# Performance work log

Hardware: AMD Instinct MI355X
Metric: run time of the kernel (lower is better)

Reference implementation:

```python
import jax, jax.numpy as jnp
import numpy as np
import math

B, L, E, H = 512, 200, 64, 4
D = E // H
NEG = jnp.float32(-(2.0 ** 32) + 1.0)


def setup_inputs() -> dict:
    key = jax.random.key(0)
    ks = jax.random.split(key, 12)
    inp = jax.random.normal(ks[0], (B, L, E), dtype=jnp.float32)
    # realistic variable-length histories: mask[b, t] = t < len_b, len_b in [1, L]
    lens = jax.random.randint(ks[1], (B, 1), 1, L + 1)
    mask = jnp.arange(L)[None, :] < lens  # [B, L] bool
    s = 1.0 / math.sqrt(E)
    pos_enc = jax.random.normal(ks[2], (1, L, E), dtype=jnp.float32)
    Wk = jax.random.uniform(ks[3], (E, E), jnp.float32, -s, s)
    bk = jnp.zeros((E,), jnp.float32)
    Wv = jax.random.uniform(ks[4], (E, E), jnp.float32, -s, s)
    bv = jnp.zeros((E,), jnp.float32)
    Wq = jax.random.uniform(ks[5], (E, E), jnp.float32, -s, s)
    bq = jnp.zeros((E,), jnp.float32)
    Wf = jax.random.uniform(ks[6], (E, E), jnp.float32, -s, s)
    bf = jnp.zeros((E,), jnp.float32)
    return {"input": inp, "mask": mask, "pos_enc": pos_enc,
            "Wk": Wk, "bk": bk, "Wv": Wv, "bv": bv,
            "Wq": Wq, "bq": bq, "Wf": Wf, "bf": bf}


def reference(input, mask, pos_enc, Wk, bk, Wv, bv, Wq, bq, Wf, bf):
    x = input + pos_enc  # [B, L, E]
    # project and split heads: [B, H, L, D]
    def split(t):
        return t.reshape(B, L, H, D).transpose(0, 2, 1, 3)
    k = split(x @ Wk.T + bk)
    v = split(x @ Wv.T + bv)
    q = split(x @ Wq.T + bq) / math.sqrt(D)
    scores = jnp.einsum('bhqd,bhkd->bhqk', q, k)  # [B, H, L, L]
    # key_mask in torch code broadcasts over dim 3 (mask on the QUERY axis),
    # query_mask is its transpose (mask on the KEY axis). Combined: both must be valid.
    both = mask[:, None, :, None] & mask[:, None, None, :]  # [B, 1, L, L]
    scores = jnp.where(both, scores, NEG)
    attn = jax.nn.softmax(scores, axis=-1)
    # dropout is identity at inference; omitted deterministically
    out = jnp.einsum('bhqk,bhkd->bhqd', attn, v)
    out = out.transpose(0, 2, 1, 3).reshape(B, L, E)
    out = out @ Wf.T + bf
    fm = mask.astype(jnp.float32)[:, :, None]  # [B, L, 1]
    lens = jnp.sum(fm, axis=1)  # [B, 1]
    pooled = jnp.sum(out * fm, axis=1) / (lens + 1e-8)  # [B, E]
    return pooled
```

## Files before the change

### kernel.cpp

```cpp
#include <hip/hip_runtime.h>
#include <hip/hip_fp16.h>
#include <math.h>

#define Bn 512
#define Ln 200
#define En 64
#define Hn 4
#define Dn 16
#define KS3 18
#define VS3 200
#define QSC 0.36067376022224085f

typedef _Float16 __f16;
typedef __fp16 fp16x2 __attribute__((ext_vector_type(2)));
typedef __f16 f16x4 __attribute__((ext_vector_type(4)));
typedef __f16 f16x8 __attribute__((ext_vector_type(8)));
typedef float f32x4 __attribute__((ext_vector_type(4)));

#if __has_builtin(__builtin_amdgcn_exp2f)
__device__ __forceinline__ float fexp2(float x) { return __builtin_amdgcn_exp2f(x); }
#else
__device__ __forceinline__ float fexp2(float x) { return exp2f(x); }
#endif

__device__ __forceinline__ f16x8 pack8s(float4 a, float4 b, float4 pa, float4 pb) {
    f16x8 r;
    r[0] = (__f16)(a.x + pa.x); r[1] = (__f16)(a.y + pa.y);
    r[2] = (__f16)(a.z + pa.z); r[3] = (__f16)(a.w + pa.w);
    r[4] = (__f16)(b.x + pb.x); r[5] = (__f16)(b.y + pb.y);
    r[6] = (__f16)(b.z + pb.z); r[7] = (__f16)(b.w + pb.w);
    return r;
}
__device__ __forceinline__ f16x8 pack8(float4 a, float4 b) {
    f16x8 r;
    r[0] = (__f16)a.x; r[1] = (__f16)a.y; r[2] = (__f16)a.z; r[3] = (__f16)a.w;
    r[4] = (__f16)b.x; r[5] = (__f16)b.y; r[6] = (__f16)b.z; r[7] = (__f16)b.w;
    return r;
}

__device__ __forceinline__ f16x4 pack4rtz(float e0, float e1, float e2, float e3) {
    const fp16x2 lo = __builtin_amdgcn_cvt_pkrtz(e0, e1);
    const fp16x2 hi = __builtin_amdgcn_cvt_pkrtz(e2, e3);
    f16x4 r;
    r[0] = (__f16)lo[0]; r[1] = (__f16)lo[1];
    r[2] = (__f16)hi[0]; r[3] = (__f16)hi[1];
    return r;
}

template<int NI>
__device__ __forceinline__ void attn_core(
    const __f16* __restrict__ Kh_, const __f16* __restrict__ Qh_, const __f16* __restrict__ Vt_,
    int qt0, int klo, int khi, int nt, int len, int quad, int ln16,
    f32x4 (&o2)[4], f32x4 (&lacc)[4])
{
    const f16x4 ones = {(__f16)1.f, (__f16)1.f, (__f16)1.f, (__f16)1.f};
    f16x4 qf[NI];
    #pragma unroll
    for (int i = 0; i < NI; ++i) {
        int qr = min((qt0 + i) * 16 + ln16, Ln - 1);
        qf[i] = *(const f16x4*)(Qh_ + qr * KS3 + quad * 4);
    }
    const bool needmask = (khi == nt);
    const int kfull = khi - (needmask ? 1 : 0);

    f16x4 kf = *(const f16x4*)(Kh_ + min(klo * 16 + ln16, Ln - 1) * KS3 + quad * 4);
    f16x4 vf = *(const f16x4*)(Vt_ + ln16 * VS3 + min(klo * 16 + quad * 4, Ln - 4));

    for (int kt = klo; kt < kfull; ++kt) {
        const int krn = min((kt + 1) * 16 + ln16, Ln - 1);
        const int vcn = min((kt + 1) * 16 + quad * 4, Ln - 4);
        const f16x4 kfn = *(const f16x4*)(Kh_ + krn * KS3 + quad * 4);
        const f16x4 vfn = *(const f16x4*)(Vt_ + ln16 * VS3 + vcn);
        f32x4 s[NI];
        #pragma unroll
        for (int i = 0; i < NI; ++i)
            s[i] = __builtin_amdgcn_mfma_f32_16x16x16f16(kf, qf[i], (f32x4){0,0,0,0}, 0, 0, 0);
        f16x4 pf[NI];
        #pragma unroll
        for (int i = 0; i < NI; ++i) {
            pf[i] = pack4rtz(fexp2(fminf(s[i][0], 14.5f)),
                             fexp2(fminf(s[i][1], 14.5f)),
                             fexp2(fminf(s[i][2], 14.5f)),
                             fexp2(fminf(s[i][3], 14.5f)));
        }
        #pragma unroll
        for (int i = 0; i < NI; ++i) {
            o2[i]   = __builtin_amdgcn_mfma_f32_16x16x16f16(vf,   pf[i], o2[i],   0, 0, 0);
            lacc[i] = __builtin_amdgcn_mfma_f32_16x16x16f16(ones, pf[i], lacc[i], 0, 0, 0);
        }
        kf = kfn; vf = vfn;
    }
    if (needmask) {
        const int kbase = (nt - 1) * 16 + quad * 4;
        f32x4 s[NI];
        #pragma unroll
        for (int i = 0; i < NI; ++i)
            s[i] = __builtin_amdgcn_mfma_f32_16x16x16f16(kf, qf[i], (f32x4){0,0,0,0}, 0, 0, 0);
        f16x4 pf[NI];
        #pragma unroll
        for (int i = 0; i < NI; ++i) {
            float e[4];
            #pragma unroll
            for (int j = 0; j < 4; ++j) {
                const bool kok = (kbase + j) < len;
                e[j] = kok ? fexp2(fminf(s[i][j], 14.5f)) : 0.f;
            }
            pf[i] = pack4rtz(e[0], e[1], e[2], e[3]);
        }
        #pragma unroll
        for (int i = 0; i < NI; ++i) {
            o2[i]   = __builtin_amdgcn_mfma_f32_16x16x16f16(vf,   pf[i], o2[i],   0, 0, 0);
            lacc[i] = __builtin_amdgcn_mfma_f32_16x16x16f16(ones, pf[i], lacc[i], 0, 0, 0);
        }
    }
}

__global__ __launch_bounds__(256, 4) void fused_kernel(
    const float* __restrict__ input, const int* __restrict__ mask,
    const float* __restrict__ pos_enc,
    const float* __restrict__ Wk, const float* __restrict__ bk,
    const float* __restrict__ Wv, const float* __restrict__ bv,
    const float* __restrict__ Wq, const float* __restrict__ bq,
    const float* __restrict__ Wf, const float* __restrict__ bf_,
    float* __restrict__ out)
{
    __shared__ __align__(16) __f16 Kh[Ln * KS3];
    __shared__ __align__(16) __f16 Qh[Ln * KS3];
    __shared__ __align__(16) __f16 Vt[16 * VS3];
    __shared__ float lred[4][4][16];
    __shared__ float red[4][16];
    __shared__ float ph[16];
    __shared__ int cnt_red[4];

    const int tid  = threadIdx.x;
    const int lin  = ((blockIdx.x & 7) << 8) | (blockIdx.x >> 3);
    const int b    = lin >> 2, h = lin & 3;
    const int wave = tid >> 6, lane = tid & 63;
    const int quad = lane >> 4, ln16 = lane & 15;

    const float4* in4 = (const float4*)(input + (size_t)b * Ln * En);
    const float4* pe4 = (const float4*)pos_enc;

    float4 px0, px1, px2, px3;
    {
        const int o4 = (wave * 16 + ln16) * 16 + quad * 2;
        px0 = in4[o4];     px1 = in4[o4 + 1];
        px2 = in4[o4 + 8]; px3 = in4[o4 + 9];
    }

    const int mv = (tid < Ln) ? mask[b * Ln + tid] : 0;

    f16x8 bfr[3][2];
    #pragma unroll
    for (int m = 0; m < 3; ++m) {
        const float* W = (m == 0) ? Wk : (m == 1) ? Wv : Wq;
        #pragma unroll
        for (int ks = 0; ks < 2; ++ks) {
            const float4* wp = (const float4*)(W + (size_t)(h * 16 + ln16) * 64) + (ks * 8 + quad * 2);
            bfr[m][ks] = pack8(wp[0], wp[1]);
        }
    }
    const int cg = h * 16 + ln16;
    const float bkv = bk[cg], bvv = bv[cg], bqv = bq[cg];

    int c = (mv != 0) ? 1 : 0;
    #pragma unroll
    for (int off = 32; off; off >>= 1) c += __shfl_down(c, off, 64);
    if (lane == 0) cnt_red[wave] = c;
    __syncthreads();
    const int len = cnt_red[0] + cnt_red[1] + cnt_red[2] + cnt_red[3];
    const int nt = (len + 15) >> 4;

    for (int rt = wave; rt < nt; rt += 4) {
        const int R = rt * 16 + ln16;
        const bool rok = (R < Ln);
        const int o4 = R * 16 + quad * 2;

        const int rtn = rt + 4;
        const int Rn = rtn * 16 + ln16;
        float4 pxn0 = {0,0,0,0}, pxn1 = {0,0,0,0}, pxn2 = {0,0,0,0}, pxn3 = {0,0,0,0};
        if (rtn < nt && Rn < Ln) {
            const int o4n = Rn * 16 + quad * 2;
            pxn0 = in4[o4n];     pxn1 = in4[o4n + 1];
            pxn2 = in4[o4n + 8]; pxn3 = in4[o4n + 9];
        }
        float4 pp0 = {0,0,0,0}, pp1 = {0,0,0,0}, pp2 = {0,0,0,0}, pp3 = {0,0,0,0};
        if (rok) {
            pp0 = pe4[o4];     pp1 = pe4[o4 + 1];
            pp2 = pe4[o4 + 8]; pp3 = pe4[o4 + 9];
        }
        f16x8 af0 = pack8s(px0, px1, pp0, pp1);
        f16x8 af1 = pack8s(px2, px3, pp2, pp3);

        f32x4 acc[3];
        #pragma unroll
        for (int m = 0; m < 3; ++m) acc[m] = (f32x4){0,0,0,0};
        #pragma unroll
        for (int m = 0; m < 3; ++m)
            acc[m] = __builtin_amdgcn_mfma_f32_16x16x32_f16(af0, bfr[m][0], acc[m], 0, 0, 0);
        #pragma unroll
        for (int m = 0; m < 3; ++m)
            acc[m] = __builtin_amdgcn_mfma_f32_16x16x32_f16(af1, bfr[m][1], acc[m], 0, 0, 0);

        #pragma unroll
        for (int j = 0; j < 4; ++j) {
            const int t = rt * 16 + quad * 4 + j;
            if (t < Ln) {
                Kh[t * KS3 + ln16] = (__f16)(acc[0][j] + bkv);
                Qh[t * KS3 + ln16] = (__f16)((acc[2][j] + bqv) * QSC);
            }
        }
        const int vc0 = rt * 16 + quad * 4;
        if (vc0 < Ln) {
            f16x4 vp;
            #pragma unroll
            for (int j = 0; j < 4; ++j) vp[j] = (__f16)(acc[1][j] + bvv);
            *(f16x4*)(Vt + ln16 * VS3 + vc0) = vp;
        }
        px0 = pxn0; px1 = pxn1; px2 = pxn2; px3 = pxn3;
    }
    __syncthreads();

    const int nquad = (nt + 3) >> 2;
    int g, kh, nkh;
    if (nquad >= 3)      { g = wave;     kh = 0;         nkh = 1; }
    else if (nquad == 2) { g = wave & 1; kh = wave >> 1; nkh = 2; }
    else                 { g = 0;        kh = wave;      nkh = 4; }
    const bool active = (g < nquad);
    const int nktp = (nt + nkh - 1) / nkh;
    const int klo = kh * nktp;
    const int khi = min(klo + nktp, nt);
    const int qt0 = 4 * g;

    f32x4 o2[4], lacc[4];
    #pragma unroll
    for (int i = 0; i < 4; ++i) { o2[i] = (f32x4){0,0,0,0}; lacc[i] = (f32x4){0,0,0,0}; }

    if (active && klo < khi) {
        const int ni = __builtin_amdgcn_readfirstlane(min(4, nt - qt0));
        switch (ni) {
            case 1:  attn_core<1>(Kh, Qh, Vt, qt0, klo, khi, nt, len, quad, ln16, o2, lacc); break;
            case 2:  attn_core<2>(Kh, Qh, Vt, qt0, klo, khi, nt, len, quad, ln16, o2, lacc); break;
            case 3:  attn_core<3>(Kh, Qh, Vt, qt0, klo, khi, nt, len, quad, ln16, o2, lacc); break;
            default: attn_core<4>(Kh, Qh, Vt, qt0, klo, khi, nt, len, quad, ln16, o2, lacc); break;
        }
    }

    float l[4];
    #pragma unroll
    for (int i = 0; i < 4; ++i) l[i] = lacc[i][0];

    if (nkh > 1) {
        if (lane < 16) {
            #pragma unroll
            for (int i = 0; i < 4; ++i) lred[wave][i][lane] = l[i];
        }
        __syncthreads();
        #pragma unroll
        for (int i = 0; i < 4; ++i) {
            if (nkh == 2) l[i] = lred[g][i][ln16] + lred[g + 2][i][ln16];
            else          l[i] = lred[0][i][ln16] + lred[1][i][ln16]
                               + lred[2][i][ln16] + lred[3][i][ln16];
        }
    }

    f32x4 pool = {0.f, 0.f, 0.f, 0.f};
    if (active) {
        #pragma unroll
        for (int i = 0; i < 4; ++i) {
            const float rs = ((qt0 + i) * 16 + ln16 < len) ? 1.f / l[i] : 0.f;
            #pragma unroll
            for (int j = 0; j < 4; ++j) pool[j] = fmaf(o2[i][j], rs, pool[j]);
        }
    }

    #pragma unroll
    for (int j = 0; j < 4; ++j) {
        #pragma unroll
        for (int off = 1; off < 16; off <<= 1) pool[j] += __shfl_xor(pool[j], off, 64);
    }
    if (ln16 == 0) {
        #pragma unroll
        for (int j = 0; j < 4; ++j) red[wave][quad * 4 + j] = pool[j];
    }
    __syncthreads();
    if (tid < 16)
        ph[tid] = (red[0][tid] + red[1][tid] + red[2][tid] + red[3][tid]) / ((float)len + 1e-8f);
    __syncthreads();

    if (tid < 64) {
        const int e = tid;
        const float* wr = Wf + (size_t)e * 64 + h * 16;
        float a = (h == 0) ? bf_[e] : 0.f;
        #pragma unroll
        for (int i = 0; i < 16; ++i) a = fmaf(wr[i], ph[i], a);
        atomicAdd(out + b * En + e, a);
    }
}

extern "C" void kernel_launch(void* const* d_in, const int* in_sizes, int n_in,
                              void* d_out, int out_size, void* d_ws, size_t ws_size,
                              hipStream_t stream) {
    const float* input   = (const float*)d_in[0];
    const int*   mask    = (const int*)  d_in[1];
    const float* pos_enc = (const float*)d_in[2];
    const float* Wk      = (const float*)d_in[3];
    const float* bk      = (const float*)d_in[4];
    const float* Wv      = (const float*)d_in[5];
    const float* bv      = (const float*)d_in[6];
    const float* Wq      = (const float*)d_in[7];
    const float* bq      = (const float*)d_in[8];
    const float* Wf      = (const float*)d_in[9];
    const float* bf      = (const float*)d_in[10];

    float* out = (float*)d_out;
    hipMemsetAsync(out, 0, (size_t)Bn * En * sizeof(float), stream);

    fused_kernel<<<Bn * Hn, 256, 0, stream>>>(input, mask, pos_enc,
                                              Wk, bk, Wv, bv, Wq, bq, Wf, bf, out);
}
```

Baseline: 122.0 us.

## Use persistent 512-thread blocks with atomic ticket work queue over (batch, head) items

Replaces the one-block-per-(batch,head) launch with 1024 persistent blocks of 8 waves that pull work items from a global atomic ticket counter. The projection loop now strides over 8 waves and attention splits key ranges across more waves, with the l-reduction always going through shared memory. The intent is to balance the very uneven per-item work caused by variable sequence lengths and to use more waves per item. In exchange it adds an atomic plus extra barriers per item, a second memset for the ticket, and possible occupancy limits from launch_bounds(512,8).

```diff
diff --git a/kernel.cpp b/kernel.cpp
--- a/kernel.cpp
+++ b/kernel.cpp
@@ -6,7 +6,7 @@
 #define Ln 200
 #define En 64
 #define Hn 4
-#define Dn 16
+#define NITEMS (Bn * Hn)
 #define KS3 18
 #define VS3 200
 #define QSC 0.36067376022224085f
@@ -115,186 +115,210 @@
     }
 }
 
-__global__ __launch_bounds__(256, 4) void fused_kernel(
+__global__ __launch_bounds__(512, 8) void fused_kernel(
     const float* __restrict__ input, const int* __restrict__ mask,
     const float* __restrict__ pos_enc,
     const float* __restrict__ Wk, const float* __restrict__ bk,
     const float* __restrict__ Wv, const float* __restrict__ bv,
     const float* __restrict__ Wq, const float* __restrict__ bq,
     const float* __restrict__ Wf, const float* __restrict__ bf_,
-    float* __restrict__ out)
+    float* __restrict__ out, int* __restrict__ ticket)
 {
     __shared__ __align__(16) __f16 Kh[Ln * KS3];
     __shared__ __align__(16) __f16 Qh[Ln * KS3];
     __shared__ __align__(16) __f16 Vt[16 * VS3];
-    __shared__ float lred[4][4][16];
-    __shared__ float red[4][16];
+    __shared__ float lred[8][4][16];
+    __shared__ float red[8][16];
     __shared__ float ph[16];
-    __shared__ int cnt_red[4];
+    __shared__ int cnt_red[8];
+    __shared__ int item_sh;
 
     const int tid  = threadIdx.x;
-    const int lin  = ((blockIdx.x & 7) << 8) | (blockIdx.x >> 3);
-    const int b    = lin >> 2, h = lin & 3;
     const int wave = tid >> 6, lane = tid & 63;
     const int quad = lane >> 4, ln16 = lane & 15;
-
-    const float4* in4 = (const float4*)(input + (size_t)b * Ln * En);
     const float4* pe4 = (const float4*)pos_enc;
 
-    float4 px0, px1, px2, px3;
-    {
-        const int o4 = (wave * 16 + ln16) * 16 + quad * 2;
-        px0 = in4[o4];     px1 = in4[o4 + 1];
-        px2 = in4[o4 + 8]; px3 = in4[o4 + 9];
-    }
-
-    const int mv = (tid < Ln) ? mask[b * Ln + tid] : 0;
-
-    f16x8 bfr[3][2];
-    #pragma unroll
-    for (int m = 0; m < 3; ++m) {
-        const float* W = (m == 0) ? Wk : (m == 1) ? Wv : Wq;
-        #pragma unroll
-        for (int ks = 0; ks < 2; ++ks) {
-            const float4* wp = (const float4*)(W + (size_t)(h * 16 + ln16) * 64) + (ks * 8 + quad * 2);
-            bfr[m][ks] = pack8(wp[0], wp[1]);
-        }
-    }
-    const int cg = h * 16 + ln16;
-    const float bkv = bk[cg], bvv = bv[cg], bqv = bq[cg];
-
-    int c = (mv != 0) ? 1 : 0;
-    #pragma unroll
-    for (int off = 32; off; off >>= 1) c += __shfl_down(c, off, 64);
-    if (lane == 0) cnt_red[wave] = c;
-    __syncthreads();
-    const int len = cnt_red[0] + cnt_red[1] + cnt_red[2] + cnt_red[3];
-    const int nt = (len + 15) >> 4;
-
-    for (int rt = wave; rt < nt; rt += 4) {
-        const int R = rt * 16 + ln16;
-        const bool rok = (R < Ln);
-        const int o4 = R * 16 + quad * 2;
-
-        const int rtn = rt + 4;
-        const int Rn = rtn * 16 + ln16;
-        float4 pxn0 = {0,0,0,0}, pxn1 = {0,0,0,0}, pxn2 = {0,0,0,0}, pxn3 = {0,0,0,0};
-        if (rtn < nt && Rn < Ln) {
-            const int o4n = Rn * 16 + quad * 2;
-            pxn0 = in4[o4n];     pxn1 = in4[o4n + 1];
-            pxn2 = in4[o4n + 8]; pxn3 = in4[o4n + 9];
-        }
-        float4 pp0 = {0,0,0,0}, pp1 = {0,0,0,0}, pp2 = {0,0,0,0}, pp3 = {0,0,0,0};
-        if (rok) {
-            pp0 = pe4[o4];     pp1 = pe4[o4 + 1];
-            pp2 = pe4[o4 + 8]; pp3 = pe4[o4 + 9];
-        }
-        f16x8 af0 = pack8s(px0, px1, pp0, pp1);
-        f16x8 af1 = pack8s(px2, px3, pp2, pp3);
-
-        f32x4 acc[3];
-        #pragma unroll
-        for (int m = 0; m < 3; ++m) acc[m] = (f32x4){0,0,0,0};
-        #pragma unroll
-        for (int m = 0; m < 3; ++m)
-            acc[m] = __builtin_amdgcn_mfma_f32_16x16x32_f16(af0, bfr[m][0], acc[m], 0, 0, 0);
-        #pragma unroll
-        for (int m = 0; m < 3; ++m)
-            acc[m] = __builtin_amdgcn_mfma_f32_16x16x32_f16(af1, bfr[m][1], acc[m], 0, 0, 0);
+    for (;;) {
+        __syncthreads();
+        if (tid == 0) item_sh = atomicAdd(ticket, 1);
+        __syncthreads();
+        const int item = item_sh;
+        if (item >= NITEMS) break;
+        const int b = item >> 2, h = item & 3;
+
+        const float4* in4 = (const float4*)(input + (size_t)b * Ln * En);
+
+        float4 px0 = {0,0,0,0}, px1 = {0,0,0,0}, px2 = {0,0,0,0}, px3 = {0,0,0,0};
+        if (wave == 0) {
+            const int o4 = ln16 * 16 + quad * 2;
+            px0 = in4[o4];     px1 = in4[o4 + 1];
+            px2 = in4[o4 + 8]; px3 = in4[o4 + 9];
+        }
+
+        const int mv = (tid < Ln) ? mask[b * Ln + tid] : 0;
+
+        f16x8 bfr[3][2];
+        #pragma unroll
+        for (int m = 0; m < 3; ++m) {
+            const float* W = (m == 0) ? Wk : (m == 1) ? Wv : Wq;
+            #pragma unroll
+            for (int ks = 0; ks < 2; ++ks) {
+                const float4* wp = (const float4*)(W + (size_t)(h * 16 + ln16) * 64) + (ks * 8 + quad * 2);
+                bfr[m][ks] = pack8(wp[0], wp[1]);
+            }
+        }
+        const int cg = h * 16 + ln16;
+        const float bkv = bk[cg], bvv = bv[cg], bqv = bq[cg];
+
+        int c = (mv != 0) ? 1 : 0;
+        #pragma unroll
+        for (int off = 32; off; off >>= 1) c += __shfl_down(c, off, 64);
+        if (lane == 0) cnt_red[wave] = c;
+        __syncthreads();
+        int len = 0;
+        #pragma unroll
+        for (int w = 0; w < 8; ++w) len += cnt_red[w];
+        const int nt = (len + 15) >> 4;
+
+        if (wave != 0 && wave < nt) {
+            const int o4 = (wave * 16 + ln16) * 16 + quad * 2;
+            px0 = in4[o4];     px1 = in4[o4 + 1];
+            px2 = in4[o4 + 8]; px3 = in4[o4 + 9];
+        }
+
+        for (int rt = wave; rt < nt; rt += 8) {
+            const int R = rt * 16 + ln16;
+            const bool rok = (R < Ln);
+            const int o4 = R * 16 + quad * 2;
+
+            const int rtn = rt + 8;
+            const int Rn = rtn * 16 + ln16;
+            float4 pxn0 = {0,0,0,0}, pxn1 = {0,0,0,0}, pxn2 = {0,0,0,0}, pxn3 = {0,0,0,0};
+            if (rtn < nt && Rn < Ln) {
+                const int o4n = Rn * 16 + quad * 2;
+                pxn0 = in4[o4n];     pxn1 = in4[o4n + 1];
+                pxn2 = in4[o4n + 8]; pxn3 = in4[o4n + 9];
+            }
+            float4 pp0 = {0,0,0,0}, pp1 = {0,0,0,0}, pp2 = {0,0,0,0}, pp3 = {0,0,0,0};
+            if (rok) {
+                pp0 = pe4[o4];     pp1 = pe4[o4 + 1];
+                pp2 = pe4[o4 + 8]; pp3 = pe4[o4 + 9];
+            }
+            const f16x8 af0 = pack8s(px0, px1, pp0, pp1);
+            const f16x8 af1 = pack8s(px2, px3, pp2, pp3);
+
+            f32x4 acc[3];
+            #pragma unroll
+            for (int m = 0; m < 3; ++m) acc[m] = (f32x4){0,0,0,0};
+            #pragma unroll
+            for (int m = 0; m < 3; ++m)
+                acc[m] = __builtin_amdgcn_mfma_f32_16x16x32_f16(af0, bfr[m][0], acc[m], 0, 0, 0);
+            #pragma unroll
+            for (int m = 0; m < 3; ++m)
+                acc[m] = __builtin_amdgcn_mfma_f32_16x16x32_f16(af1, bfr[m][1], acc[m], 0, 0, 0);
+
+            #pragma unroll
+            for (int j = 0; j < 4; ++j) {
+                const int t = rt * 16 + quad * 4 + j;
+                if (t < Ln) {
+                    Kh[t * KS3 + ln16] = (__f16)(acc[0][j] + bkv);
+                    Qh[t * KS3 + ln16] = (__f16)((acc[2][j] + bqv) * QSC);
+                }
+            }
+            const int vc0 = rt * 16 + quad * 4;
+            if (vc0 < Ln) {
+                f16x4 vp;
+                #pragma unroll
+                for (int j = 0; j < 4; ++j) vp[j] = (__f16)(acc[1][j] + bvv);
+                *(f16x4*)(Vt + ln16 * VS3 + vc0) = vp;
+            }
+            px0 = pxn0; px1 = pxn1; px2 = pxn2; px3 = pxn3;
+        }
+        __syncthreads();
+
+        const int nquad = (nt + 3) >> 2;
+        int g, kh, nkh;
+        if (nquad >= 3)      { g = wave & 3; kh = wave >> 2; nkh = 2; }
+        else if (nquad == 2) { g = wave & 1; kh = wave >> 1; nkh = 4; }
+        else                 { g = 0;        kh = wave;      nkh = 8; }
+        const bool active = (g < nquad);
+        const int nktp = (nt + nkh - 1) / nkh;
+        const int klo = kh * nktp;
+        const int khi = min(klo + nktp, nt);
+        const int qt0 = 4 * g;
+
+        f32x4 o2[4], lacc[4];
+        #pragma unroll
+        for (int i = 0; i < 4; ++i) { o2[i] = (f32x4){0,0,0,0}; lacc[i] = (f32x4){0,0,0,0}; }
+
+        if (active && klo < khi) {
+            const int ni = __builtin_amdgcn_readfirstlane(min(4, nt - qt0));
+            switch (ni) {
+                case 1:  attn_core<1>(Kh, Qh, Vt, qt0, klo, khi, nt, len, quad, ln16, o2, lacc); break;
+                case 2:  attn_core<2>(Kh, Qh, Vt, qt0, klo, khi, nt, len, quad, ln16, o2, lacc); break;
+                case 3:  attn_core<3>(Kh, Qh, Vt, qt0, klo, khi, nt, len, quad, ln16, o2, lacc); break;
+                default: attn_core<4>(Kh, Qh, Vt, qt0, klo, khi, nt, len, quad, ln16, o2, lacc); break;
+            }
+        }
+
+        float l[4];
+        #pragma unroll
+        for (int i = 0; i < 4; ++i) l[i] = lacc[i][0];
+
+        if (lane < 16) {
+            #pragma unroll
+            for (int i = 0; i < 4; ++i) lred[wave][i][lane] = l[i];
+        }
+        __syncthreads();
+        #pragma unroll
+        for (int i = 0; i < 4; ++i) {
+            if (nkh == 2)      l[i] = lred[g][i][ln16] + lred[g + 4][i][ln16];
+            else if (nkh == 4) l[i] = lred[g][i][ln16] + lred[g + 2][i][ln16]
+                                    + lred[g + 4][i][ln16] + lred[g + 6][i][ln16];
+            else {
+                float s = 0.f;
+                #pragma unroll
+                for (int w = 0; w < 8; ++w) s += lred[w][i][ln16];
+                l[i] = s;
+            }
+        }
+
+        f32x4 pool = {0.f, 0.f, 0.f, 0.f};
+        if (active) {
+            #pragma unroll
+            for (int i = 0; i < 4; ++i) {
+                const float rs = ((qt0 + i) * 16 + ln16 < len) ? 1.f / l[i] : 0.f;
+                #pragma unroll
+                for (int j = 0; j < 4; ++j) pool[j] = fmaf(o2[i][j], rs, pool[j]);
+            }
+        }
 
         #pragma unroll
         for (int j = 0; j < 4; ++j) {
-            const int t = rt * 16 + quad * 4 + j;
-            if (t < Ln) {
-                Kh[t * KS3 + ln16] = (__f16)(acc[0][j] + bkv);
-                Qh[t * KS3 + ln16] = (__f16)((acc[2][j] + bqv) * QSC);
-            }
-        }
-        const int vc0 = rt * 16 + quad * 4;
-        if (vc0 < Ln) {
-            f16x4 vp;
-            #pragma unroll
-            for (int j = 0; j < 4; ++j) vp[j] = (__f16)(acc[1][j] + bvv);
-            *(f16x4*)(Vt + ln16 * VS3 + vc0) = vp;
-        }
-        px0 = pxn0; px1 = pxn1; px2 = pxn2; px3 = pxn3;
-    }
-    __syncthreads();
-
-    const int nquad = (nt + 3) >> 2;
-    int g, kh, nkh;
-    if (nquad >= 3)      { g = wave;     kh = 0;         nkh = 1; }
-    else if (nquad == 2) { g = wave & 1; kh = wave >> 1; nkh = 2; }
-    else                 { g = 0;        kh = wave;      nkh = 4; }
-    const bool active = (g < nquad);
-    const int nktp = (nt + nkh - 1) / nkh;
-    const int klo = kh * nktp;
-    const int khi = min(klo + nktp, nt);
-    const int qt0 = 4 * g;
-
-    f32x4 o2[4], lacc[4];
-    #pragma unroll
-    for (int i = 0; i < 4; ++i) { o2[i] = (f32x4){0,0,0,0}; lacc[i] = (f32x4){0,0,0,0}; }
-
-    if (active && klo < khi) {
-        const int ni = __builtin_amdgcn_readfirstlane(min(4, nt - qt0));
-        switch (ni) {
-            case 1:  attn_core<1>(Kh, Qh, Vt, qt0, klo, khi, nt, len, quad, ln16, o2, lacc); break;
-            case 2:  attn_core<2>(Kh, Qh, Vt, qt0, klo, khi, nt, len, quad, ln16, o2, lacc); break;
-            case 3:  attn_core<3>(Kh, Qh, Vt, qt0, klo, khi, nt, len, quad, ln16, o2, lacc); break;
-            default: attn_core<4>(Kh, Qh, Vt, qt0, klo, khi, nt, len, quad, ln16, o2, lacc); break;
-        }
-    }
-
-    float l[4];
-    #pragma unroll
-    for (int i = 0; i < 4; ++i) l[i] = lacc[i][0];
-
-    if (nkh > 1) {
-        if (lane < 16) {
-            #pragma unroll
-            for (int i = 0; i < 4; ++i) lred[wave][i][lane] = l[i];
-        }
-        __syncthreads();
-        #pragma unroll
-        for (int i = 0; i < 4; ++i) {
-            if (nkh == 2) l[i] = lred[g][i][ln16] + lred[g + 2][i][ln16];
-            else          l[i] = lred[0][i][ln16] + lred[1][i][ln16]
-                               + lred[2][i][ln16] + lred[3][i][ln16];
-        }
-    }
-
-    f32x4 pool = {0.f, 0.f, 0.f, 0.f};
-    if (active) {
-        #pragma unroll
-        for (int i = 0; i < 4; ++i) {
-            const float rs = ((qt0 + i) * 16 + ln16 < len) ? 1.f / l[i] : 0.f;
-            #pragma unroll
-            for (int j = 0; j < 4; ++j) pool[j] = fmaf(o2[i][j], rs, pool[j]);
-        }
-    }
-
-    #pragma unroll
-    for (int j = 0; j < 4; ++j) {
-        #pragma unroll
-        for (int off = 1; off < 16; off <<= 1) pool[j] += __shfl_xor(pool[j], off, 64);
-    }
-    if (ln16 == 0) {
-        #pragma unroll
-        for (int j = 0; j < 4; ++j) red[wave][quad * 4 + j] = pool[j];
-    }
-    __syncthreads();
-    if (tid < 16)
-        ph[tid] = (red[0][tid] + red[1][tid] + red[2][tid] + red[3][tid]) / ((float)len + 1e-8f);
-    __syncthreads();
-
-    if (tid < 64) {
-        const int e = tid;
-        const float* wr = Wf + (size_t)e * 64 + h * 16;
-        float a = (h == 0) ? bf_[e] : 0.f;
-        #pragma unroll
-        for (int i = 0; i < 16; ++i) a = fmaf(wr[i], ph[i], a);
-        atomicAdd(out + b * En + e, a);
+            #pragma unroll
+            for (int off = 1; off < 16; off <<= 1) pool[j] += __shfl_xor(pool[j], off, 64);
+        }
+        if (ln16 == 0) {
+            #pragma unroll
+            for (int j = 0; j < 4; ++j) red[wave][quad * 4 + j] = pool[j];
+        }
+        __syncthreads();
+        if (tid < 16) {
+            float s = 0.f;
+            #pragma unroll
+            for (int w = 0; w < 8; ++w) s += red[w][tid];
+            ph[tid] = s / ((float)len + 1e-8f);
+        }
+        __syncthreads();
+
+        if (tid < 64) {
+            const int e = tid;
+            const float* wr = Wf + (size_t)e * 64 + h * 16;
+            float a = (h == 0) ? bf_[e] : 0.f;
+            #pragma unroll
+            for (int i = 0; i < 16; ++i) a = fmaf(wr[i], ph[i], a);
+            atomicAdd(out + b * En + e, a);
+        }
     }
 }
 
@@ -313,9 +337,13 @@
     const float* Wf      = (const float*)d_in[9];
     const float* bf      = (const float*)d_in[10];
 
-    float* out = (float*)d_out;
+    float* out    = (float*)d_out;
+    int*   ticket = (int*)d_ws;
+
     hipMemsetAsync(out, 0, (size_t)Bn * En * sizeof(float), stream);
-
-    fused_kernel<<<Bn * Hn, 256, 0, stream>>>(input, mask, pos_enc,
-                                              Wk, bk, Wv, bv, Wq, bq, Wf, bf, out);
-}
+    hipMemsetAsync(ticket, 0, 64, stream);
+
+    fused_kernel<<<1024, 512, 0, stream>>>(input, mask, pos_enc,
+                                           Wk, bk, Wv, bv, Wq, bq, Wf, bf,
+                                           out, ticket);
+}
```

Result: slower. 214.7 us (+76.0%).

## Convert to persistent blocks pulling (batch, head) items from an atomic ticket

Applied to the files above, without the earlier changes.

Replaces the one-block-per-(batch,head) grid with a fixed grid of 1792 persistent blocks. Each block repeatedly grabs a work item through an atomic counter in workspace, which is zeroed by an extra memset. Dynamic scheduling is meant to balance the uneven per-item cost from variable sequence lengths and to cut block launch overhead. Input prefetch for waves beyond the valid tile count is now deferred until the length is known. The cost is an extra memset, a global atomic and barrier per item, and an extra trailing barrier per iteration.

```diff
diff --git a/kernel.cpp b/kernel.cpp
--- a/kernel.cpp
+++ b/kernel.cpp
@@ -6,7 +6,7 @@
 #define Ln 200
 #define En 64
 #define Hn 4
-#define Dn 16
+#define NITEMS (Bn * Hn)
 #define KS3 18
 #define VS3 200
 #define QSC 0.36067376022224085f
@@ -122,7 +122,7 @@
     const float* __restrict__ Wv, const float* __restrict__ bv,
     const float* __restrict__ Wq, const float* __restrict__ bq,
     const float* __restrict__ Wf, const float* __restrict__ bf_,
-    float* __restrict__ out)
+    float* __restrict__ out, int* __restrict__ ticket)
 {
     __shared__ __align__(16) __f16 Kh[Ln * KS3];
     __shared__ __align__(16) __f16 Qh[Ln * KS3];
@@ -131,170 +131,184 @@
     __shared__ float red[4][16];
     __shared__ float ph[16];
     __shared__ int cnt_red[4];
+    __shared__ int item_sh;
 
     const int tid  = threadIdx.x;
-    const int lin  = ((blockIdx.x & 7) << 8) | (blockIdx.x >> 3);
-    const int b    = lin >> 2, h = lin & 3;
     const int wave = tid >> 6, lane = tid & 63;
     const int quad = lane >> 4, ln16 = lane & 15;
-
-    const float4* in4 = (const float4*)(input + (size_t)b * Ln * En);
     const float4* pe4 = (const float4*)pos_enc;
 
-    float4 px0, px1, px2, px3;
-    {
-        const int o4 = (wave * 16 + ln16) * 16 + quad * 2;
-        px0 = in4[o4];     px1 = in4[o4 + 1];
-        px2 = in4[o4 + 8]; px3 = in4[o4 + 9];
-    }
-
-    const int mv = (tid < Ln) ? mask[b * Ln + tid] : 0;
-
-    f16x8 bfr[3][2];
-    #pragma unroll
-    for (int m = 0; m < 3; ++m) {
-        const float* W = (m == 0) ? Wk : (m == 1) ? Wv : Wq;
-        #pragma unroll
-        for (int ks = 0; ks < 2; ++ks) {
-            const float4* wp = (const float4*)(W + (size_t)(h * 16 + ln16) * 64) + (ks * 8 + quad * 2);
-            bfr[m][ks] = pack8(wp[0], wp[1]);
-        }
-    }
-    const int cg = h * 16 + ln16;
-    const float bkv = bk[cg], bvv = bv[cg], bqv = bq[cg];
-
-    int c = (mv != 0) ? 1 : 0;
-    #pragma unroll
-    for (int off = 32; off; off >>= 1) c += __shfl_down(c, off, 64);
-    if (lane == 0) cnt_red[wave] = c;
-    __syncthreads();
-    const int len = cnt_red[0] + cnt_red[1] + cnt_red[2] + cnt_red[3];
-    const int nt = (len + 15) >> 4;
-
-    for (int rt = wave; rt < nt; rt += 4) {
-        const int R = rt * 16 + ln16;
-        const bool rok = (R < Ln);
-        const int o4 = R * 16 + quad * 2;
-
-        const int rtn = rt + 4;
-        const int Rn = rtn * 16 + ln16;
-        float4 pxn0 = {0,0,0,0}, pxn1 = {0,0,0,0}, pxn2 = {0,0,0,0}, pxn3 = {0,0,0,0};
-        if (rtn < nt && Rn < Ln) {
-            const int o4n = Rn * 16 + quad * 2;
-            pxn0 = in4[o4n];     pxn1 = in4[o4n + 1];
-            pxn2 = in4[o4n + 8]; pxn3 = in4[o4n + 9];
-        }
-        float4 pp0 = {0,0,0,0}, pp1 = {0,0,0,0}, pp2 = {0,0,0,0}, pp3 = {0,0,0,0};
-        if (rok) {
-            pp0 = pe4[o4];     pp1 = pe4[o4 + 1];
-            pp2 = pe4[o4 + 8]; pp3 = pe4[o4 + 9];
-        }
-        f16x8 af0 = pack8s(px0, px1, pp0, pp1);
-        f16x8 af1 = pack8s(px2, px3, pp2, pp3);
-
-        f32x4 acc[3];
-        #pragma unroll
-        for (int m = 0; m < 3; ++m) acc[m] = (f32x4){0,0,0,0};
-        #pragma unroll
-        for (int m = 0; m < 3; ++m)
-            acc[m] = __builtin_amdgcn_mfma_f32_16x16x32_f16(af0, bfr[m][0], acc[m], 0, 0, 0);
-        #pragma unroll
-        for (int m = 0; m < 3; ++m)
-            acc[m] = __builtin_amdgcn_mfma_f32_16x16x32_f16(af1, bfr[m][1], acc[m], 0, 0, 0);
+    for (;;) {
+        if (tid == 0) item_sh = atomicAdd(ticket, 1);
+        __syncthreads();
+        const int item = item_sh;
+        if (item >= NITEMS) break;
+        const int b = item >> 2, h = item & 3;
+
+        const float4* in4 = (const float4*)(input + (size_t)b * Ln * En);
+
+        float4 px0 = {0,0,0,0}, px1 = {0,0,0,0}, px2 = {0,0,0,0}, px3 = {0,0,0,0};
+        if (wave == 0) {
+            const int o4 = ln16 * 16 + quad * 2;
+            px0 = in4[o4];     px1 = in4[o4 + 1];
+            px2 = in4[o4 + 8]; px3 = in4[o4 + 9];
+        }
+
+        const int mv = (tid < Ln) ? mask[b * Ln + tid] : 0;
+
+        f16x8 bfr[3][2];
+        #pragma unroll
+        for (int m = 0; m < 3; ++m) {
+            const float* W = (m == 0) ? Wk : (m == 1) ? Wv : Wq;
+            #pragma unroll
+            for (int ks = 0; ks < 2; ++ks) {
+                const float4* wp = (const float4*)(W + (size_t)(h * 16 + ln16) * 64) + (ks * 8 + quad * 2);
+                bfr[m][ks] = pack8(wp[0], wp[1]);
+            }
+        }
+        const int cg = h * 16 + ln16;
+        const float bkv = bk[cg], bvv = bv[cg], bqv = bq[cg];
+
+        int c = (mv != 0) ? 1 : 0;
+        #pragma unroll
+        for (int off = 32; off; off >>= 1) c += __shfl_down(c, off, 64);
+        if (lane == 0) cnt_red[wave] = c;
+        __syncthreads();
+        const int len = cnt_red[0] + cnt_red[1] + cnt_red[2] + cnt_red[3];
+        const int nt = (len + 15) >> 4;
+
+        if (wave != 0 && wave < nt) {
+            const int o4 = (wave * 16 + ln16) * 16 + quad * 2;
+            px0 = in4[o4];     px1 = in4[o4 + 1];
+            px2 = in4[o4 + 8]; px3 = in4[o4 + 9];
+        }
+
+        for (int rt = wave; rt < nt; rt += 4) {
+            const int R = rt * 16 + ln16;
+            const bool rok = (R < Ln);
+            const int o4 = R * 16 + quad * 2;
+
+            const int rtn = rt + 4;
+            const int Rn = rtn * 16 + ln16;
+            float4 pxn0 = {0,0,0,0}, pxn1 = {0,0,0,0}, pxn2 = {0,0,0,0}, pxn3 = {0,0,0,0};
+            if (rtn < nt && Rn < Ln) {
+                const int o4n = Rn * 16 + quad * 2;
+                pxn0 = in4[o4n];     pxn1 = in4[o4n + 1];
+                pxn2 = in4[o4n + 8]; pxn3 = in4[o4n + 9];
+            }
+            float4 pp0 = {0,0,0,0}, pp1 = {0,0,0,0}, pp2 = {0,0,0,0}, pp3 = {0,0,0,0};
+            if (rok) {
+                pp0 = pe4[o4];     pp1 = pe4[o4 + 1];
+                pp2 = pe4[o4 + 8]; pp3 = pe4[o4 + 9];
+            }
+            const f16x8 af0 = pack8s(px0, px1, pp0, pp1);
+            const f16x8 af1 = pack8s(px2, px3, pp2, pp3);
+
+            f32x4 acc[3];
+            #pragma unroll
+            for (int m = 0; m < 3; ++m) acc[m] = (f32x4){0,0,0,0};
+            #pragma unroll
+            for (int m = 0; m < 3; ++m)
+                acc[m] = __builtin_amdgcn_mfma_f32_16x16x32_f16(af0, bfr[m][0], acc[m], 0, 0, 0);
+            #pragma unroll
+            for (int m = 0; m < 3; ++m)
+                acc[m] = __builtin_amdgcn_mfma_f32_16x16x32_f16(af1, bfr[m][1], acc[m], 0, 0, 0);
+
+            #pragma unroll
+            for (int j = 0; j < 4; ++j) {
+                const int t = rt * 16 + quad * 4 + j;
+                if (t < Ln) {
+                    Kh[t * KS3 + ln16] = (__f16)(acc[0][j] + bkv);
+                    Qh[t * KS3 + ln16] = (__f16)((acc[2][j] + bqv) * QSC);
+                }
+            }
+            const int vc0 = rt * 16 + quad * 4;
+            if (vc0 < Ln) {
+                f16x4 vp;
+                #pragma unroll
+                for (int j = 0; j < 4; ++j) vp[j] = (__f16)(acc[1][j] + bvv);
+                *(f16x4*)(Vt + ln16 * VS3 + vc0) = vp;
+            }
+            px0 = pxn0; px1 = pxn1; px2 = pxn2; px3 = pxn3;
+        }
+        __syncthreads();
+
+        const int nquad = (nt + 3) >> 2;
+        int g, kh, nkh;
+        if (nquad >= 3)      { g = wave;     kh = 0;         nkh = 1; }
+        else if (nquad == 2) { g = wave & 1; kh = wave >> 1; nkh = 2; }
+        else                 { g = 0;        kh = wave;      nkh = 4; }
+        const bool active = (g < nquad);
+        const int nktp = (nt + nkh - 1) / nkh;
+        const int klo = kh * nktp;
+        const int khi = min(klo + nktp, nt);
+        const int qt0 = 4 * g;
+
+        f32x4 o2[4], lacc[4];
+        #pragma unroll
+        for (int i = 0; i < 4; ++i) { o2[i] = (f32x4){0,0,0,0}; lacc[i] = (f32x4){0,0,0,0}; }
+
+        if (active && klo < khi) {
+            const int ni = __builtin_amdgcn_readfirstlane(min(4, nt - qt0));
+            switch (ni) {
+                case 1:  attn_core<1>(Kh, Qh, Vt, qt0, klo, khi, nt, len, quad, ln16, o2, lacc); break;
+                case 2:  attn_core<2>(Kh, Qh, Vt, qt0, klo, khi, nt, len, quad, ln16, o2, lacc); break;
+                case 3:  attn_core<3>(Kh, Qh, Vt, qt0, klo, khi, nt, len, quad, ln16, o2, lacc); break;
+                default: attn_core<4>(Kh, Qh, Vt, qt0, klo, khi, nt, len, quad, ln16, o2, lacc); break;
+            }
+        }
+
+        float l[4];
+        #pragma unroll
+        for (int i = 0; i < 4; ++i) l[i] = lacc[i][0];
+
+        if (nkh > 1) {
+            if (lane < 16) {
+                #pragma unroll
+                for (int i = 0; i < 4; ++i) lred[wave][i][lane] = l[i];
+            }
+            __syncthreads();
+            #pragma unroll
+            for (int i = 0; i < 4; ++i) {
+                if (nkh == 2) l[i] = lred[g][i][ln16] + lred[g + 2][i][ln16];
+                else          l[i] = lred[0][i][ln16] + lred[1][i][ln16]
+                                   + lred[2][i][ln16] + lred[3][i][ln16];
+            }
+        }
+
+        f32x4 pool = {0.f, 0.f, 0.f, 0.f};
+        if (active) {
+            #pragma unroll
+            for (int i = 0; i < 4; ++i) {
+                const float rs = ((qt0 + i) * 16 + ln16 < len) ? 1.f / l[i] : 0.f;
+                #pragma unroll
+                for (int j = 0; j < 4; ++j) pool[j] = fmaf(o2[i][j], rs, pool[j]);
+            }
+        }
 
         #pragma unroll
         for (int j = 0; j < 4; ++j) {
-            const int t = rt * 16 + quad * 4 + j;
-            if (t < Ln) {
-                Kh[t * KS3 + ln16] = (__f16)(acc[0][j] + bkv);
-                Qh[t * KS3 + ln16] = (__f16)((acc[2][j] + bqv) * QSC);
-            }
-        }
-        const int vc0 = rt * 16 + quad * 4;
-        if (vc0 < Ln) {
-            f16x4 vp;
-            #pragma unroll
-            for (int j = 0; j < 4; ++j) vp[j] = (__f16)(acc[1][j] + bvv);
-            *(f16x4*)(Vt + ln16 * VS3 + vc0) = vp;
-        }
-        px0 = pxn0; px1 = pxn1; px2 = pxn2; px3 = pxn3;
-    }
-    __syncthreads();
-
-    const int nquad = (nt + 3) >> 2;
-    int g, kh, nkh;
-    if (nquad >= 3)      { g = wave;     kh = 0;         nkh = 1; }
-    else if (nquad == 2) { g = wave & 1; kh = wave >> 1; nkh = 2; }
-    else                 { g = 0;        kh = wave;      nkh = 4; }
-    const bool active = (g < nquad);
-    const int nktp = (nt + nkh - 1) / nkh;
-    const int klo = kh * nktp;
-    const int khi = min(klo + nktp, nt);
-    const int qt0 = 4 * g;
-
-    f32x4 o2[4], lacc[4];
-    #pragma unroll
-    for (int i = 0; i < 4; ++i) { o2[i] = (f32x4){0,0,0,0}; lacc[i] = (f32x4){0,0,0,0}; }
-
-    if (active && klo < khi) {
-        const int ni = __builtin_amdgcn_readfirstlane(min(4, nt - qt0));
-        switch (ni) {
-            case 1:  attn_core<1>(Kh, Qh, Vt, qt0, klo, khi, nt, len, quad, ln16, o2, lacc); break;
-            case 2:  attn_core<2>(Kh, Qh, Vt, qt0, klo, khi, nt, len, quad, ln16, o2, lacc); break;
-            case 3:  attn_core<3>(Kh, Qh, Vt, qt0, klo, khi, nt, len, quad, ln16, o2, lacc); break;
-            default: attn_core<4>(Kh, Qh, Vt, qt0, klo, khi, nt, len, quad, ln16, o2, lacc); break;
-        }
-    }
-
-    float l[4];
-    #pragma unroll
-    for (int i = 0; i < 4; ++i) l[i] = lacc[i][0];
-
-    if (nkh > 1) {
-        if (lane < 16) {
-            #pragma unroll
-            for (int i = 0; i < 4; ++i) lred[wave][i][lane] = l[i];
-        }
-        __syncthreads();
-        #pragma unroll
-        for (int i = 0; i < 4; ++i) {
-            if (nkh == 2) l[i] = lred[g][i][ln16] + lred[g + 2][i][ln16];
-            else          l[i] = lred[0][i][ln16] + lred[1][i][ln16]
-                               + lred[2][i][ln16] + lred[3][i][ln16];
-        }
-    }
-
-    f32x4 pool = {0.f, 0.f, 0.f, 0.f};
-    if (active) {
-        #pragma unroll
-        for (int i = 0; i < 4; ++i) {
-            const float rs = ((qt0 + i) * 16 + ln16 < len) ? 1.f / l[i] : 0.f;
-            #pragma unroll
-            for (int j = 0; j < 4; ++j) pool[j] = fmaf(o2[i][j], rs, pool[j]);
-        }
-    }
-
-    #pragma unroll
-    for (int j = 0; j < 4; ++j) {
-        #pragma unroll
-        for (int off = 1; off < 16; off <<= 1) pool[j] += __shfl_xor(pool[j], off, 64);
-    }
-    if (ln16 == 0) {
-        #pragma unroll
-        for (int j = 0; j < 4; ++j) red[wave][quad * 4 + j] = pool[j];
-    }
-    __syncthreads();
-    if (tid < 16)
-        ph[tid] = (red[0][tid] + red[1][tid] + red[2][tid] + red[3][tid]) / ((float)len + 1e-8f);
-    __syncthreads();
-
-    if (tid < 64) {
-        const int e = tid;
-        const float* wr = Wf + (size_t)e * 64 + h * 16;
-        float a = (h == 0) ? bf_[e] : 0.f;
-        #pragma unroll
-        for (int i = 0; i < 16; ++i) a = fmaf(wr[i], ph[i], a);
-        atomicAdd(out + b * En + e, a);
+            #pragma unroll
+            for (int off = 1; off < 16; off <<= 1) pool[j] += __shfl_xor(pool[j], off, 64);
+        }
+        if (ln16 == 0) {
+            #pragma unroll
+            for (int j = 0; j < 4; ++j) red[wave][quad * 4 + j] = pool[j];
+        }
+        __syncthreads();
+        if (tid < 16)
+            ph[tid] = (red[0][tid] + red[1][tid] + red[2][tid] + red[3][tid]) / ((float)len + 1e-8f);
+        __syncthreads();
+
+        if (tid < 64) {
+            const int e = tid;
+            const float* wr = Wf + (size_t)e * 64 + h * 16;
+            float a = (h == 0) ? bf_[e] : 0.f;
+            #pragma unroll
+            for (int i = 0; i < 16; ++i) a = fmaf(wr[i], ph[i], a);
+            atomicAdd(out + b * En + e, a);
+        }
+        __syncthreads();
     }
 }
 
@@ -313,9 +327,13 @@
     const float* Wf      = (const float*)d_in[9];
     const float* bf      = (const float*)d_in[10];
 
-    float* out = (float*)d_out;
+    float* out    = (float*)d_out;
+    int*   ticket = (int*)d_ws;
+
     hipMemsetAsync(out, 0, (size_t)Bn * En * sizeof(float), stream);
-
-    fused_kernel<<<Bn * Hn, 256, 0, stream>>>(input, mask, pos_enc,
-                                              Wk, bk, Wv, bv, Wq, bq, Wf, bf, out);
-}
+    hipMemsetAsync(ticket, 0, 64, stream);
+
+    fused_kernel<<<1792, 256, 0, stream>>>(input, mask, pos_enc,
+                                           Wk, bk, Wv, bv, Wq, bq, Wf, bf,
+                                           out, ticket);
+}
```

Result: slower. 146.6 us (+20.2%).

## Process one batch per block with one wave per head, dropping atomics and memset

Applied to the files above, without the earlier changes.

Blocks now cover a whole batch element instead of one (batch, head) pair. The input is read once, and all four heads' K/Q/V are projected together into per-head shared arrays, with biases folded into the accumulator init. Each wave then runs attention for its own head over all query groups, which removes the key-split and l-reduction syncs. Output is written directly after an in-block reduction, so the atomics and the memset launch are gone. The trade-offs are fewer blocks (512), more shared memory and registers per block (launch bounds lowered to 2), and no key-split parallelism for short sequences.

```diff
diff --git a/kernel.cpp b/kernel.cpp
--- a/kernel.cpp
+++ b/kernel.cpp
@@ -6,9 +6,8 @@
 #define Ln 200
 #define En 64
 #define Hn 4
-#define Dn 16
-#define KS3 18
-#define VS3 200
+#define KS 16
+#define VS 200
 #define QSC 0.36067376022224085f
 
 typedef _Float16 __f16;
@@ -50,7 +49,7 @@
 template<int NI>
 __device__ __forceinline__ void attn_core(
     const __f16* __restrict__ Kh_, const __f16* __restrict__ Qh_, const __f16* __restrict__ Vt_,
-    int qt0, int klo, int khi, int nt, int len, int quad, int ln16,
+    int qt0, int nt, int len, int quad, int ln16,
     f32x4 (&o2)[4], f32x4 (&lacc)[4])
 {
     const f16x4 ones = {(__f16)1.f, (__f16)1.f, (__f16)1.f, (__f16)1.f};
@@ -58,19 +57,18 @@
     #pragma unroll
     for (int i = 0; i < NI; ++i) {
         int qr = min((qt0 + i) * 16 + ln16, Ln - 1);
-        qf[i] = *(const f16x4*)(Qh_ + qr * KS3 + quad * 4);
-    }
-    const bool needmask = (khi == nt);
-    const int kfull = khi - (needmask ? 1 : 0);
-
-    f16x4 kf = *(const f16x4*)(Kh_ + min(klo * 16 + ln16, Ln - 1) * KS3 + quad * 4);
-    f16x4 vf = *(const f16x4*)(Vt_ + ln16 * VS3 + min(klo * 16 + quad * 4, Ln - 4));
-
-    for (int kt = klo; kt < kfull; ++kt) {
+        qf[i] = *(const f16x4*)(Qh_ + qr * KS + quad * 4);
+    }
+    const int kfull = nt - 1;
+
+    f16x4 kf = *(const f16x4*)(Kh_ + ln16 * KS + quad * 4);
+    f16x4 vf = *(const f16x4*)(Vt_ + ln16 * VS + quad * 4);
+
+    for (int kt = 0; kt < kfull; ++kt) {
         const int krn = min((kt + 1) * 16 + ln16, Ln - 1);
         const int vcn = min((kt + 1) * 16 + quad * 4, Ln - 4);
-        const f16x4 kfn = *(const f16x4*)(Kh_ + krn * KS3 + quad * 4);
-        const f16x4 vfn = *(const f16x4*)(Vt_ + ln16 * VS3 + vcn);
+        const f16x4 kfn = *(const f16x4*)(Kh_ + krn * KS + quad * 4);
+        const f16x4 vfn = *(const f16x4*)(Vt_ + ln16 * VS + vcn);
         f32x4 s[NI];
         #pragma unroll
         for (int i = 0; i < NI; ++i)
@@ -90,7 +88,7 @@
         }
         kf = kfn; vf = vfn;
     }
-    if (needmask) {
+    {
         const int kbase = (nt - 1) * 16 + quad * 4;
         f32x4 s[NI];
         #pragma unroll
@@ -115,7 +113,7 @@
     }
 }
 
-__global__ __launch_bounds__(256, 4) void fused_kernel(
+__global__ __launch_bounds__(256, 2) void fused_kernel(
     const float* __restrict__ input, const int* __restrict__ mask,
     const float* __restrict__ pos_enc,
     const float* __restrict__ Wk, const float* __restrict__ bk,
@@ -124,54 +122,60 @@
     const float* __restrict__ Wf, const float* __restrict__ bf_,
     float* __restrict__ out)
 {
-    __shared__ __align__(16) __f16 Kh[Ln * KS3];
-    __shared__ __align__(16) __f16 Qh[Ln * KS3];
-    __shared__ __align__(16) __f16 Vt[16 * VS3];
-    __shared__ float lred[4][4][16];
-    __shared__ float red[4][16];
-    __shared__ float ph[16];
-    __shared__ int cnt_red[4];
+    __shared__ __align__(16) __f16 KhA[Hn][Ln * KS];
+    __shared__ __align__(16) __f16 QhA[Hn][Ln * KS];
+    __shared__ __align__(16) __f16 VtA[Hn][16 * VS];
+    __shared__ float swr[4][16];
+    __shared__ float ared[4][64];
 
     const int tid  = threadIdx.x;
-    const int lin  = ((blockIdx.x & 7) << 8) | (blockIdx.x >> 3);
-    const int b    = lin >> 2, h = lin & 3;
-    const int wave = tid >> 6, lane = tid & 63;
+    const int b    = blockIdx.x;
+    const int wv   = tid >> 6, lane = tid & 63;
     const int quad = lane >> 4, ln16 = lane & 15;
 
     const float4* in4 = (const float4*)(input + (size_t)b * Ln * En);
     const float4* pe4 = (const float4*)pos_enc;
 
-    float4 px0, px1, px2, px3;
-    {
-        const int o4 = (wave * 16 + ln16) * 16 + quad * 2;
+    float4 px0 = {0,0,0,0}, px1 = {0,0,0,0}, px2 = {0,0,0,0}, px3 = {0,0,0,0};
+    if (wv == 0) {
+        const int o4 = ln16 * 16 + quad * 2;
         px0 = in4[o4];     px1 = in4[o4 + 1];
         px2 = in4[o4 + 8]; px3 = in4[o4 + 9];
     }
 
-    const int mv = (tid < Ln) ? mask[b * Ln + tid] : 0;
-
-    f16x8 bfr[3][2];
+    const int* mb = mask + b * Ln;
+    int c = (mb[lane] != 0) + (mb[64 + lane] != 0) + (mb[128 + lane] != 0)
+          + ((lane < Ln - 192) ? (mb[192 + lane] != 0) : 0);
+
+    f16x8 bfr[3][4][2];
+    float bz[3][4];
     #pragma unroll
     for (int m = 0; m < 3; ++m) {
         const float* W = (m == 0) ? Wk : (m == 1) ? Wv : Wq;
-        #pragma unroll
-        for (int ks = 0; ks < 2; ++ks) {
-            const float4* wp = (const float4*)(W + (size_t)(h * 16 + ln16) * 64) + (ks * 8 + quad * 2);
-            bfr[m][ks] = pack8(wp[0], wp[1]);
-        }
-    }
-    const int cg = h * 16 + ln16;
-    const float bkv = bk[cg], bvv = bv[cg], bqv = bq[cg];
-
-    int c = (mv != 0) ? 1 : 0;
+        const float* B = (m == 0) ? bk : (m == 1) ? bv : bq;
+        #pragma unroll
+        for (int h = 0; h < 4; ++h) {
+            #pragma unroll
+            for (int ks = 0; ks < 2; ++ks) {
+                const float4* wp = (const float4*)(W + (size_t)(h * 16 + ln16) * 64) + (ks * 8 + quad * 2);
+                bfr[m][h][ks] = pack8(wp[0], wp[1]);
+            }
+            bz[m][h] = B[h * 16 + ln16];
+        }
+    }
+
     #pragma unroll
     for (int off = 32; off; off >>= 1) c += __shfl_down(c, off, 64);
-    if (lane == 0) cnt_red[wave] = c;
-    __syncthreads();
-    const int len = cnt_red[0] + cnt_red[1] + cnt_red[2] + cnt_red[3];
+    const int len = __shfl(c, 0, 64);
     const int nt = (len + 15) >> 4;
 
-    for (int rt = wave; rt < nt; rt += 4) {
+    if (wv != 0 && wv < nt) {
+        const int o4 = (wv * 16 + ln16) * 16 + quad * 2;
+        px0 = in4[o4];     px1 = in4[o4 + 1];
+        px2 = in4[o4 + 8]; px3 = in4[o4 + 9];
+    }
+
+    for (int rt = wv; rt < nt; rt += 4) {
         const int R = rt * 16 + ln16;
         const bool rok = (R < Ln);
         const int o4 = R * 16 + quad * 2;
@@ -189,86 +193,72 @@
             pp0 = pe4[o4];     pp1 = pe4[o4 + 1];
             pp2 = pe4[o4 + 8]; pp3 = pe4[o4 + 9];
         }
-        f16x8 af0 = pack8s(px0, px1, pp0, pp1);
-        f16x8 af1 = pack8s(px2, px3, pp2, pp3);
-
-        f32x4 acc[3];
-        #pragma unroll
-        for (int m = 0; m < 3; ++m) acc[m] = (f32x4){0,0,0,0};
+        const f16x8 af0 = pack8s(px0, px1, pp0, pp1);
+        const f16x8 af1 = pack8s(px2, px3, pp2, pp3);
+
+        f32x4 acc[3][4];
         #pragma unroll
         for (int m = 0; m < 3; ++m)
-            acc[m] = __builtin_amdgcn_mfma_f32_16x16x32_f16(af0, bfr[m][0], acc[m], 0, 0, 0);
+            #pragma unroll
+            for (int h = 0; h < 4; ++h)
+                acc[m][h] = (f32x4){bz[m][h], bz[m][h], bz[m][h], bz[m][h]};
         #pragma unroll
         for (int m = 0; m < 3; ++m)
-            acc[m] = __builtin_amdgcn_mfma_f32_16x16x32_f16(af1, bfr[m][1], acc[m], 0, 0, 0);
+            #pragma unroll
+            for (int h = 0; h < 4; ++h)
+                acc[m][h] = __builtin_amdgcn_mfma_f32_16x16x32_f16(af0, bfr[m][h][0], acc[m][h], 0, 0, 0);
+        #pragma unroll
+        for (int m = 0; m < 3; ++m)
+            #pragma unroll
+            for (int h = 0; h < 4; ++h)
+                acc[m][h] = __builtin_amdgcn_mfma_f32_16x16x32_f16(af1, bfr[m][h][1], acc[m][h], 0, 0, 0);
 
         #pragma unroll
         for (int j = 0; j < 4; ++j) {
             const int t = rt * 16 + quad * 4 + j;
             if (t < Ln) {
-                Kh[t * KS3 + ln16] = (__f16)(acc[0][j] + bkv);
-                Qh[t * KS3 + ln16] = (__f16)((acc[2][j] + bqv) * QSC);
+                #pragma unroll
+                for (int h = 0; h < 4; ++h) {
+                    KhA[h][t * KS + ln16] = (__f16)acc[0][h][j];
+                    QhA[h][t * KS + ln16] = (__f16)(acc[2][h][j] * QSC);
+                }
             }
         }
         const int vc0 = rt * 16 + quad * 4;
         if (vc0 < Ln) {
-            f16x4 vp;
-            #pragma unroll
-            for (int j = 0; j < 4; ++j) vp[j] = (__f16)(acc[1][j] + bvv);
-            *(f16x4*)(Vt + ln16 * VS3 + vc0) = vp;
+            #pragma unroll
+            for (int h = 0; h < 4; ++h) {
+                f16x4 vp;
+                #pragma unroll
+                for (int j = 0; j < 4; ++j) vp[j] = (__f16)acc[1][h][j];
+                *(f16x4*)(&VtA[h][ln16 * VS + vc0]) = vp;
+            }
         }
         px0 = pxn0; px1 = pxn1; px2 = pxn2; px3 = pxn3;
     }
     __syncthreads();
 
+    const __f16* Kh_ = KhA[wv];
+    const __f16* Qh_ = QhA[wv];
+    const __f16* Vt_ = VtA[wv];
     const int nquad = (nt + 3) >> 2;
-    int g, kh, nkh;
-    if (nquad >= 3)      { g = wave;     kh = 0;         nkh = 1; }
-    else if (nquad == 2) { g = wave & 1; kh = wave >> 1; nkh = 2; }
-    else                 { g = 0;        kh = wave;      nkh = 4; }
-    const bool active = (g < nquad);
-    const int nktp = (nt + nkh - 1) / nkh;
-    const int klo = kh * nktp;
-    const int khi = min(klo + nktp, nt);
-    const int qt0 = 4 * g;
-
-    f32x4 o2[4], lacc[4];
-    #pragma unroll
-    for (int i = 0; i < 4; ++i) { o2[i] = (f32x4){0,0,0,0}; lacc[i] = (f32x4){0,0,0,0}; }
-
-    if (active && klo < khi) {
+
+    f32x4 pool = {0.f, 0.f, 0.f, 0.f};
+    for (int g = 0; g < nquad; ++g) {
+        const int qt0 = 4 * g;
+        f32x4 o2[4], lacc[4];
+        #pragma unroll
+        for (int i = 0; i < 4; ++i) { o2[i] = (f32x4){0,0,0,0}; lacc[i] = (f32x4){0,0,0,0}; }
         const int ni = __builtin_amdgcn_readfirstlane(min(4, nt - qt0));
         switch (ni) {
-            case 1:  attn_core<1>(Kh, Qh, Vt, qt0, klo, khi, nt, len, quad, ln16, o2, lacc); break;
-            case 2:  attn_core<2>(Kh, Qh, Vt, qt0, klo, khi, nt, len, quad, ln16, o2, lacc); break;
-            case 3:  attn_core<3>(Kh, Qh, Vt, qt0, klo, khi, nt, len, quad, ln16, o2, lacc); break;
-            default: attn_core<4>(Kh, Qh, Vt, qt0, klo, khi, nt, len, quad, ln16, o2, lacc); break;
-        }
-    }
-
-    float l[4];
-    #pragma unroll
-    for (int i = 0; i < 4; ++i) l[i] = lacc[i][0];
-
-    if (nkh > 1) {
-        if (lane < 16) {
-            #pragma unroll
-            for (int i = 0; i < 4; ++i) lred[wave][i][lane] = l[i];
-        }
-        __syncthreads();
+            case 1:  attn_core<1>(Kh_, Qh_, Vt_, qt0, nt, len, quad, ln16, o2, lacc); break;
+            case 2:  attn_core<2>(Kh_, Qh_, Vt_, qt0, nt, len, quad, ln16, o2, lacc); break;
+            case 3:  attn_core<3>(Kh_, Qh_, Vt_, qt0, nt, len, quad, ln16, o2, lacc); break;
+            default: attn_core<4>(Kh_, Qh_, Vt_, qt0, nt, len, quad, ln16, o2, lacc); break;
+        }
         #pragma unroll
         for (int i = 0; i < 4; ++i) {
-            if (nkh == 2) l[i] = lred[g][i][ln16] + lred[g + 2][i][ln16];
-            else          l[i] = lred[0][i][ln16] + lred[1][i][ln16]
-                               + lred[2][i][ln16] + lred[3][i][ln16];
-        }
-    }
-
-    f32x4 pool = {0.f, 0.f, 0.f, 0.f};
-    if (active) {
-        #pragma unroll
-        for (int i = 0; i < 4; ++i) {
-            const float rs = ((qt0 + i) * 16 + ln16 < len) ? 1.f / l[i] : 0.f;
+            const float rs = ((qt0 + i) * 16 + ln16 < len) ? 1.f / lacc[i][0] : 0.f;
             #pragma unroll
             for (int j = 0; j < 4; ++j) pool[j] = fmaf(o2[i][j], rs, pool[j]);
         }
@@ -281,21 +271,22 @@
     }
     if (ln16 == 0) {
         #pragma unroll
-        for (int j = 0; j < 4; ++j) red[wave][quad * 4 + j] = pool[j];
-    }
+        for (int j = 0; j < 4; ++j) swr[wv][quad * 4 + j] = pool[j];
+    }
+    float phv[16];
+    #pragma unroll
+    for (int i = 0; i < 16; ++i) phv[i] = swr[wv][i];
+
+    const float invlen = 1.f / ((float)len + 1e-8f);
+    const float* wr = Wf + (size_t)lane * En + wv * 16;
+    float a = 0.f;
+    #pragma unroll
+    for (int i = 0; i < 16; ++i) a = fmaf(wr[i], phv[i], a);
+    ared[wv][lane] = a * invlen;
     __syncthreads();
-    if (tid < 16)
-        ph[tid] = (red[0][tid] + red[1][tid] + red[2][tid] + red[3][tid]) / ((float)len + 1e-8f);
-    __syncthreads();
-
-    if (tid < 64) {
-        const int e = tid;
-        const float* wr = Wf + (size_t)e * 64 + h * 16;
-        float a = (h == 0) ? bf_[e] : 0.f;
-        #pragma unroll
-        for (int i = 0; i < 16; ++i) a = fmaf(wr[i], ph[i], a);
-        atomicAdd(out + b * En + e, a);
-    }
+
+    if (tid < 64)
+        out[b * En + tid] = bf_[tid] + ared[0][tid] + ared[1][tid] + ared[2][tid] + ared[3][tid];
 }
 
 extern "C" void kernel_launch(void* const* d_in, const int* in_sizes, int n_in,
@@ -314,8 +305,7 @@
     const float* bf      = (const float*)d_in[10];
 
     float* out = (float*)d_out;
-    hipMemsetAsync(out, 0, (size_t)Bn * En * sizeof(float), stream);
-
-    fused_kernel<<<Bn * Hn, 256, 0, stream>>>(input, mask, pos_enc,
-                                              Wk, bk, Wv, bv, Wq, bq, Wf, bf, out);
-}
+
+    fused_kernel<<<Bn, 256, 0, stream>>>(input, mask, pos_enc,
+                                         Wk, bk, Wv, bv, Wq, bq, Wf, bf, out);
+}
```

After: 125.2 us. 1.03x slower.
